# Kernel optimization log

Hardware: AMD Instinct MI355X
Metric: run time of the kernel (lower is better)

The kernel has to match this reference:

```python
import jax, jax.numpy as jnp
import numpy as np

N_NODES = 100000
N_EDGES = 600000
PRE = 128
NEXT = 128


def setup_inputs() -> dict:
    key = jax.random.key(0)
    k1, k2, k3, k4, k5, k6 = jax.random.split(key, 6)
    node_embedding = jax.random.normal(k1, (N_NODES, PRE), dtype=jnp.float32)
    edges = jax.random.randint(k2, (N_EDGES, 2), 0, N_NODES, dtype=jnp.int64)
    # Linear weights use torch convention [out, in]; scale ~ He-ish for sanity.
    s = 1.0 / np.sqrt(PRE)
    W_left = jax.random.normal(k3, (NEXT, PRE), dtype=jnp.float32) * s
    W_right = jax.random.normal(k4, (NEXT, PRE), dtype=jnp.float32) * s
    W_update = jax.random.normal(k5, (NEXT, PRE), dtype=jnp.float32) * s
    b_update = jax.random.normal(k6, (NEXT,), dtype=jnp.float32) * s
    return {
        "node_embedding": node_embedding,
        "edges": edges,
        "W_left": W_left,
        "W_right": W_right,
        "W_update": W_update,
        "b_update": b_update,
        "next_size": NEXT,
    }


def reference(node_embedding, edges, W_left, W_right, W_update, b_update, next_size):
    # Vectorized form of the per-edge loop:
    #   for each edge (i0, i1):
    #     lg  = sigmoid(W_l @ x[i0])
    #     rg  = sigmoid(W_r @ x[i1])
    #     mid = tanh(W_u @ (x[i0] + x[i1]) + b)
    #     out = lg*mid + rg*mid
    x0 = node_embedding[edges[:, 0]]  # [E, pre]
    x1 = node_embedding[edges[:, 1]]  # [E, pre]
    lg = jax.nn.sigmoid(jnp.einsum("ep,np->en", x0, W_left))
    rg = jax.nn.sigmoid(jnp.einsum("ep,np->en", x1, W_right))
    mid = jnp.tanh(jnp.einsum("ep,np->en", x0 + x1, W_update) + b_update)
    return (lg + rg) * mid  # [E, next]
```

## Files before the change

kernel.cpp:

```cpp
#include <hip/hip_runtime.h>
#include <hip/hip_bf16.h>

typedef __attribute__((ext_vector_type(8))) short short8;
typedef __attribute__((ext_vector_type(4))) float f32x4;

__device__ __forceinline__ float bflo(unsigned int u) { return __uint_as_float(u << 16); }
__device__ __forceinline__ float bfhi(unsigned int u) { return __uint_as_float(u & 0xffff0000u); }
__device__ __forceinline__ unsigned int bfrne(float f) {
    unsigned int u = __float_as_uint(f);
    return (u + 0x7fffu + ((u >> 16) & 1u)) >> 16;
}
__device__ __forceinline__ unsigned int packbf2(float lo, float hi) {
    return (bfrne(lo) & 0xffffu) | (bfrne(hi) << 16);
}
__device__ __forceinline__ float fast_rcp(float x) { return __builtin_amdgcn_rcpf(x); }
__device__ __forceinline__ float sigmoidf_fast(float x) { return fast_rcp(1.0f + __expf(-x)); }
__device__ __forceinline__ float tanhf_fast(float x) {
    float e = __expf(2.0f * x);
    return 1.0f - 2.0f * fast_rcp(e + 1.0f);
}
__device__ __forceinline__ short8 pack8(const float* f) {
    short8 r;
#pragma unroll
    for (int i = 0; i < 8; i += 2) {
        unsigned int p = packbf2(f[i], f[i + 1]);
        r[i] = (short)(p & 0xffffu);
        r[i + 1] = (short)(p >> 16);
    }
    return r;
}
__device__ __forceinline__ void unpack8(uint4 v, float* f) {
    const unsigned int* p = (const unsigned int*)&v;
#pragma unroll
    for (int j = 0; j < 4; ++j) { f[2 * j] = bflo(p[j]); f[2 * j + 1] = bfhi(p[j]); }
}

__global__ void sniff_kernel(const unsigned short* __restrict__ emb,
                             const int* __restrict__ e32, int* __restrict__ flags)
{
    __shared__ int s_f32, s_nz;
    const int t = threadIdx.x;
    if (t == 0) { s_f32 = 0; s_nz = 0; }
    __syncthreads();
    int bad = 0;
#pragma unroll 4
    for (int j = 0; j < 64; ++j) {
        unsigned int u = emb[t * 64 + j];
        if (((u >> 7) & 0xFFu) == 0xFFu) bad = 1;
    }
    int nz = 0;
#pragma unroll
    for (int j = 0; j < 8; ++j)
        if (e32[(t * 8 + j) * 2 + 1] != 0) nz = 1;
    if (bad) atomicOr(&s_f32, 1);
    if (nz) atomicOr(&s_nz, 1);
    __syncthreads();
    if (t == 0) { flags[0] = s_f32; flags[1] = s_nz ? 0 : 1; }
}

__global__ __launch_bounds__(256, 2)
void proj_kernel(const void* __restrict__ embv,
                 const void* __restrict__ w0v, const void* __restrict__ w1v,
                 const void* __restrict__ w2v,
                 unsigned short* __restrict__ SLp,
                 unsigned short* __restrict__ SRp,
                 float* __restrict__ Up,
                 const int* __restrict__ flags, int n_nodes)
{
    const int in_f32 = flags[0];
    const int w = blockIdx.y;
    const void* Wv = (w == 0) ? w0v : (w == 1 ? w1v : w2v);
    const int m0 = blockIdx.x * 128;

    __shared__ unsigned short lds[128 * 136];

    const int tid  = threadIdx.x;
    const int lane = tid & 63;
    const int wave = tid >> 6;
    const int wm   = wave & 1;
    const int wn   = wave >> 1;
    const int l15  = lane & 15;
    const int lgp  = lane >> 4;

    short8 bf[4][4];
    if (in_f32) {
        const float* W = (const float*)Wv;
#pragma unroll
        for (int nj = 0; nj < 4; ++nj) {
            const float* wrow = W + (size_t)(wn * 64 + nj * 16 + l15) * 128 + lgp * 8;
#pragma unroll
            for (int s = 0; s < 4; ++s) {
                float f[8];
                *(uint4*)&f[0] = *(const uint4*)(wrow + s * 32);
                *(uint4*)&f[4] = *(const uint4*)(wrow + s * 32 + 4);
                bf[s][nj] = pack8(f);
            }
        }
    } else {
        const unsigned short* W = (const unsigned short*)Wv;
#pragma unroll
        for (int nj = 0; nj < 4; ++nj) {
            const unsigned short* wrow = W + (size_t)(wn * 64 + nj * 16 + l15) * 128 + lgp * 8;
#pragma unroll
            for (int s = 0; s < 4; ++s)
                bf[s][nj] = *(const short8*)(wrow + s * 32);
        }
    }

    if (in_f32) {
        const float* emb = (const float*)embv;
#pragma unroll
        for (int it = 0; it < 8; ++it) {
            int i = tid + it * 256;
            int row = i >> 4, ch = i & 15;
            int g = m0 + row;
            float f[8] = {0.f, 0.f, 0.f, 0.f, 0.f, 0.f, 0.f, 0.f};
            if (g < n_nodes) {
                const float* src = emb + (size_t)g * 128 + ch * 8;
                *(uint4*)&f[0] = *(const uint4*)src;
                *(uint4*)&f[4] = *(const uint4*)(src + 4);
            }
            *(short8*)(&lds[row * 136 + ch * 8]) = pack8(f);
        }
    } else {
        const unsigned short* emb = (const unsigned short*)embv;
#pragma unroll
        for (int it = 0; it < 4; ++it) {
            int i = tid + it * 256;
            int row = i >> 3, ch = i & 7;
            int g = m0 + row;
            uint4 v = make_uint4(0u, 0u, 0u, 0u);
            if (g < n_nodes) v = *(const uint4*)(emb + (size_t)g * 128 + ch * 8);
            *(uint4*)(&lds[row * 136 + ch * 8]) = v;
        }
    }

    f32x4 acc[4][4];
#pragma unroll
    for (int mi = 0; mi < 4; ++mi)
#pragma unroll
        for (int nj = 0; nj < 4; ++nj)
            acc[mi][nj] = (f32x4){0.f, 0.f, 0.f, 0.f};

    __syncthreads();

#pragma unroll
    for (int s = 0; s < 4; ++s) {
        short8 af[4];
#pragma unroll
        for (int mi = 0; mi < 4; ++mi)
            af[mi] = *(const short8*)(&lds[(wm * 64 + mi * 16 + l15) * 136 + s * 32 + lgp * 8]);
#pragma unroll
        for (int mi = 0; mi < 4; ++mi)
#pragma unroll
            for (int nj = 0; nj < 4; ++nj)
                acc[mi][nj] = __builtin_amdgcn_mfma_f32_16x16x32_bf16(
                    af[mi], bf[s][nj], acc[mi][nj], 0, 0, 0);
    }

    if (w < 2) {
        unsigned short* out = (w == 0) ? SLp : SRp;
        const bool odd = (lane & 1);
#pragma unroll
        for (int mi = 0; mi < 4; ++mi) {
            int nodeBase = m0 + wm * 64 + mi * 16 + lgp * 4;
#pragma unroll
            for (int nj = 0; nj < 4; ++nj) {
                float v0 = sigmoidf_fast(acc[mi][nj][0]);
                float v1 = sigmoidf_fast(acc[mi][nj][1]);
                float v2 = sigmoidf_fast(acc[mi][nj][2]);
                float v3 = sigmoidf_fast(acc[mi][nj][3]);
                float p0 = __shfl_xor(v0, 1), p1 = __shfl_xor(v1, 1);
                float p2 = __shfl_xor(v2, 1), p3 = __shfl_xor(v3, 1);
                unsigned int pkA, pkB; int rA, rB;
                if (!odd) { pkA = packbf2(v0, p0); rA = 0; pkB = packbf2(v1, p1); rB = 1; }
                else      { pkA = packbf2(p2, v2); rA = 2; pkB = packbf2(p3, v3); rB = 3; }
                int colE = wn * 64 + nj * 16 + (l15 & ~1);
                int na = nodeBase + rA, nb = nodeBase + rB;
                if (na < n_nodes) *(unsigned int*)(out + (size_t)na * 128 + colE) = pkA;
                if (nb < n_nodes) *(unsigned int*)(out + (size_t)nb * 128 + colE) = pkB;
            }
        }
    } else {
#pragma unroll
        for (int mi = 0; mi < 4; ++mi) {
            int nodeBase = m0 + wm * 64 + mi * 16 + lgp * 4;
#pragma unroll
            for (int nj = 0; nj < 4; ++nj) {
                int col = wn * 64 + nj * 16 + l15;
#pragma unroll
                for (int r = 0; r < 4; ++r) {
                    int row = nodeBase + r;
                    if (row < n_nodes) Up[(size_t)row * 128 + col] = acc[mi][nj][r];
                }
            }
        }
    }
}

__global__ __launch_bounds__(256)
void edge_kernel(const int* __restrict__ e32,
                 const unsigned short* __restrict__ SL,
                 const unsigned short* __restrict__ SR,
                 const float* __restrict__ U,
                 const void* __restrict__ biasv,
                 void* __restrict__ outv,
                 const int* __restrict__ flags, int n_edges)
{
    const int in_f32 = flags[0];
    const int i64    = flags[1];
    const int tid = threadIdx.x;
    const int e = blockIdx.x * 16 + (tid >> 4);
    if (e >= n_edges) return;
    const int c = (tid & 15) * 8;

    int a, b;
    if (i64) { a = e32[4 * (size_t)e]; b = e32[4 * (size_t)e + 2]; }
    else     { a = e32[2 * (size_t)e]; b = e32[2 * (size_t)e + 1]; }

    float slf[8], srf[8], uaf[8], ubf[8], bif[8];
    unpack8(*(const uint4*)(SL + (size_t)a * 128 + c), slf);
    unpack8(*(const uint4*)(SR + (size_t)b * 128 + c), srf);
    const float* ua = U + (size_t)a * 128 + c;
    const float* ub = U + (size_t)b * 128 + c;
    *(uint4*)&uaf[0] = *(const uint4*)ua;
    *(uint4*)&uaf[4] = *(const uint4*)(ua + 4);
    *(uint4*)&ubf[0] = *(const uint4*)ub;
    *(uint4*)&ubf[4] = *(const uint4*)(ub + 4);
    if (in_f32) {
        const float* bp = (const float*)biasv + c;
        *(uint4*)&bif[0] = *(const uint4*)bp;
        *(uint4*)&bif[4] = *(const uint4*)(bp + 4);
    } else {
        unpack8(*(const uint4*)((const unsigned short*)biasv + c), bif);
    }

    float o[8];
#pragma unroll
    for (int j = 0; j < 8; ++j) {
        float s = slf[j] + srf[j];
        float x = uaf[j] + ubf[j] + bif[j];
        o[j] = s * tanhf_fast(x);
    }

    if (in_f32) {
        float* op = (float*)outv + (size_t)e * 128 + c;
        *(uint4*)op = *(const uint4*)&o[0];
        *(uint4*)(op + 4) = *(const uint4*)&o[4];
    } else {
        unsigned int res[4];
#pragma unroll
        for (int j = 0; j < 4; ++j) res[j] = packbf2(o[2 * j], o[2 * j + 1]);
        *(uint4*)((unsigned short*)outv + (size_t)e * 128 + c) = *(const uint4*)res;
    }
}

extern "C" void kernel_launch(void* const* d_in, const int* in_sizes, int n_in,
                              void* d_out, int out_size, void* d_ws, size_t ws_size,
                              hipStream_t stream)
{
    const void* emb   = d_in[0];
    const int*  edges = (const int*)d_in[1];
    const void* Wl    = d_in[2];
    const void* Wr    = d_in[3];
    const void* Wu    = d_in[4];
    const void* bias  = d_in[5];

    const int n_nodes = in_sizes[0] / 128;
    const int n_edges = in_sizes[1] / 2;

    int* flags = (int*)d_ws;
    const size_t plane_elems = (size_t)n_nodes * 128;
    unsigned short* SLp = (unsigned short*)((char*)d_ws + 256);
    unsigned short* SRp = SLp + plane_elems;
    float*          Up  = (float*)(SRp + plane_elems);

    sniff_kernel<<<1, 256, 0, stream>>>((const unsigned short*)emb, edges, flags);

    dim3 g1((n_nodes + 127) / 128, 3);
    proj_kernel<<<g1, 256, 0, stream>>>(emb, Wl, Wr, Wu, SLp, SRp, Up, flags, n_nodes);

    int g2 = (n_edges + 15) / 16;
    edge_kernel<<<g2, 256, 0, stream>>>(edges, SLp, SRp, Up, bias, d_out, flags, n_edges);
}
```

Baseline: 511.1 us.

## Store U plane in fp16, fuse three projections per block, split-bf16 activations

```diff
diff --git a/kernel.cpp b/kernel.cpp
--- a/kernel.cpp
+++ b/kernel.cpp
@@ -1,5 +1,6 @@
 #include <hip/hip_runtime.h>
 #include <hip/hip_bf16.h>
+#include <hip/hip_fp16.h>
 
 typedef __attribute__((ext_vector_type(8))) short short8;
 typedef __attribute__((ext_vector_type(4))) float f32x4;
@@ -13,26 +14,41 @@
 __device__ __forceinline__ unsigned int packbf2(float lo, float hi) {
     return (bfrne(lo) & 0xffffu) | (bfrne(hi) << 16);
 }
+__device__ __forceinline__ short8 pack8(const float* f) {
+    short8 r;
+#pragma unroll
+    for (int i = 0; i < 8; i += 2) {
+        unsigned int p = packbf2(f[i], f[i + 1]);
+        r[i] = (short)(p & 0xffffu);
+        r[i + 1] = (short)(p >> 16);
+    }
+    return r;
+}
+__device__ __forceinline__ void unpackbf8(uint4 v, float* f) {
+    const unsigned int* p = (const unsigned int*)&v;
+#pragma unroll
+    for (int j = 0; j < 4; ++j) { f[2 * j] = bflo(p[j]); f[2 * j + 1] = bfhi(p[j]); }
+}
+
+__device__ __forceinline__ unsigned int packh2(float lo, float hi) {
+    unsigned int a = __half_as_ushort(__float2half_rn(lo));
+    unsigned int b = __half_as_ushort(__float2half_rn(hi));
+    return a | (b << 16);
+}
+__device__ __forceinline__ void unpackh8(uint4 v, float* f) {
+    const unsigned int* p = (const unsigned int*)&v;
+#pragma unroll
+    for (int j = 0; j < 4; ++j) {
+        f[2 * j]     = __half2float(__ushort_as_half((unsigned short)(p[j] & 0xffffu)));
+        f[2 * j + 1] = __half2float(__ushort_as_half((unsigned short)(p[j] >> 16)));
+    }
+}
+
 __device__ __forceinline__ float fast_rcp(float x) { return __builtin_amdgcn_rcpf(x); }
 __device__ __forceinline__ float sigmoidf_fast(float x) { return fast_rcp(1.0f + __expf(-x)); }
 __device__ __forceinline__ float tanhf_fast(float x) {
     float e = __expf(2.0f * x);
     return 1.0f - 2.0f * fast_rcp(e + 1.0f);
-}
-__device__ __forceinline__ short8 pack8(const float* f) {
-    short8 r;
-#pragma unroll
-    for (int i = 0; i < 8; i += 2) {
-        unsigned int p = packbf2(f[i], f[i + 1]);
-        r[i] = (short)(p & 0xffffu);
-        r[i + 1] = (short)(p >> 16);
-    }
-    return r;
-}
-__device__ __forceinline__ void unpack8(uint4 v, float* f) {
-    const unsigned int* p = (const unsigned int*)&v;
-#pragma unroll
-    for (int j = 0; j < 4; ++j) { f[2 * j] = bflo(p[j]); f[2 * j + 1] = bfhi(p[j]); }
 }
 
 __global__ void sniff_kernel(const unsigned short* __restrict__ emb,
@@ -58,21 +74,49 @@
     if (t == 0) { flags[0] = s_f32; flags[1] = s_nz ? 0 : 1; }
 }
 
+__global__ __launch_bounds__(256)
+void prep_kernel(const void* __restrict__ w0v, const void* __restrict__ w1v,
+                 const void* __restrict__ w2v,
+                 unsigned short* __restrict__ Wb, const int* __restrict__ flags)
+{
+    const int in_f32 = flags[0];
+    const int w = blockIdx.x;
+    const void* Wv = (w == 0) ? w0v : (w == 1 ? w1v : w2v);
+    unsigned short* dst = Wb + w * 16384;
+    const int tid = threadIdx.x;
+    if (in_f32) {
+        const float* W = (const float*)Wv;
+#pragma unroll
+        for (int it = 0; it < 8; ++it) {
+            int i = (tid + it * 256) * 8;
+            float f[8];
+            *(uint4*)&f[0] = *(const uint4*)(W + i);
+            *(uint4*)&f[4] = *(const uint4*)(W + i + 4);
+            *(short8*)(dst + i) = pack8(f);
+        }
+    } else {
+        const unsigned short* W = (const unsigned short*)Wv;
+#pragma unroll
+        for (int it = 0; it < 8; ++it) {
+            int i = (tid + it * 256) * 8;
+            *(uint4*)(dst + i) = *(const uint4*)(W + i);
+        }
+    }
+}
+
 __global__ __launch_bounds__(256, 2)
 void proj_kernel(const void* __restrict__ embv,
-                 const void* __restrict__ w0v, const void* __restrict__ w1v,
-                 const void* __restrict__ w2v,
+                 const unsigned short* __restrict__ Wb,
                  unsigned short* __restrict__ SLp,
                  unsigned short* __restrict__ SRp,
-                 float* __restrict__ Up,
+                 unsigned short* __restrict__ Up,
                  const int* __restrict__ flags, int n_nodes)
 {
     const int in_f32 = flags[0];
-    const int w = blockIdx.y;
-    const void* Wv = (w == 0) ? w0v : (w == 1 ? w1v : w2v);
     const int m0 = blockIdx.x * 128;
 
-    __shared__ unsigned short lds[128 * 136];
+    __shared__ unsigned short ldsh[128 * 136];
+    __shared__ unsigned short ldsl[128 * 136];
 
     const int tid  = threadIdx.x;
     const int lane = tid & 63;
@@ -81,31 +125,6 @@
     const int wn   = wave >> 1;
     const int l15  = lane & 15;
     const int lgp  = lane >> 4;
-
-    short8 bf[4][4];
-    if (in_f32) {
-        const float* W = (const float*)Wv;
-#pragma unroll
-        for (int nj = 0; nj < 4; ++nj) {
-            const float* wrow = W + (size_t)(wn * 64 + nj * 16 + l15) * 128 + lgp * 8;
-#pragma unroll
-            for (int s = 0; s < 4; ++s) {
-                float f[8];
-                *(uint4*)&f[0] = *(const uint4*)(wrow + s * 32);
-                *(uint4*)&f[4] = *(const uint4*)(wrow + s * 32 + 4);
-                bf[s][nj] = pack8(f);
-            }
-        }
-    } else {
-        const unsigned short* W = (const unsigned short*)Wv;
-#pragma unroll
-        for (int nj = 0; nj < 4; ++nj) {
-            const unsigned short* wrow = W + (size_t)(wn * 64 + nj * 16 + l15) * 128 + lgp * 8;
-#pragma unroll
-            for (int s = 0; s < 4; ++s)
-                bf[s][nj] = *(const short8*)(wrow + s * 32);
-        }
-    }
 
     if (in_f32) {
         const float* emb = (const float*)embv;
@@ -120,7 +139,16 @@
                 *(uint4*)&f[0] = *(const uint4*)src;
                 *(uint4*)&f[4] = *(const uint4*)(src + 4);
             }
-            *(short8*)(&lds[row * 136 + ch * 8]) = pack8(f);
+            short8 h, l;
+#pragma unroll
+            for (int j = 0; j < 8; ++j) {
+                unsigned int uh = bfrne(f[j]);
+                h[j] = (short)uh;
+                float r = f[j] - __uint_as_float(uh << 16);
+                l[j] = (short)bfrne(r);
+            }
+            *(short8*)(&ldsh[row * 136 + ch * 8]) = h;
+            *(short8*)(&ldsl[row * 136 + ch * 8]) = l;
         }
     } else {
         const unsigned short* emb = (const unsigned short*)embv;
@@ -131,70 +159,85 @@
             int g = m0 + row;
             uint4 v = make_uint4(0u, 0u, 0u, 0u);
             if (g < n_nodes) v = *(const uint4*)(emb + (size_t)g * 128 + ch * 8);
-            *(uint4*)(&lds[row * 136 + ch * 8]) = v;
-        }
-    }
-
-    f32x4 acc[4][4];
-#pragma unroll
-    for (int mi = 0; mi < 4; ++mi)
-#pragma unroll
-        for (int nj = 0; nj < 4; ++nj)
-            acc[mi][nj] = (f32x4){0.f, 0.f, 0.f, 0.f};
+            *(uint4*)(&ldsh[row * 136 + ch * 8]) = v;
+        }
+    }
 
     __syncthreads();
 
-#pragma unroll
-    for (int s = 0; s < 4; ++s) {
-        short8 af[4];
+#pragma unroll 1
+    for (int w = 0; w < 3; ++w) {
+        const unsigned short* Wp = Wb + w * 16384;
+
+        short8 bf[4][4];
+#pragma unroll
+        for (int nj = 0; nj < 4; ++nj) {
+            const unsigned short* wrow = Wp + (size_t)(wn * 64 + nj * 16 + l15) * 128 + lgp * 8;
+#pragma unroll
+            for (int s = 0; s < 4; ++s)
+                bf[s][nj] = *(const short8*)(wrow + s * 32);
+        }
+
+        f32x4 acc[4][4];
 #pragma unroll
         for (int mi = 0; mi < 4; ++mi)
-            af[mi] = *(const short8*)(&lds[(wm * 64 + mi * 16 + l15) * 136 + s * 32 + lgp * 8]);
-#pragma unroll
-        for (int mi = 0; mi < 4; ++mi)
 #pragma unroll
             for (int nj = 0; nj < 4; ++nj)
-                acc[mi][nj] = __builtin_amdgcn_mfma_f32_16x16x32_bf16(
-                    af[mi], bf[s][nj], acc[mi][nj], 0, 0, 0);
-    }
-
-    if (w < 2) {
-        unsigned short* out = (w == 0) ? SLp : SRp;
+                acc[mi][nj] = (f32x4){0.f, 0.f, 0.f, 0.f};
+
+#pragma unroll
+        for (int s = 0; s < 4; ++s) {
+            short8 afh[4];
+#pragma unroll
+            for (int mi = 0; mi < 4; ++mi)
+                afh[mi] = *(const short8*)(&ldsh[(wm * 64 + mi * 16 + l15) * 136 + s * 32 + lgp * 8]);
+#pragma unroll
+            for (int mi = 0; mi < 4; ++mi)
+#pragma unroll
+                for (int nj = 0; nj < 4; ++nj)
+                    acc[mi][nj] = __builtin_amdgcn_mfma_f32_16x16x32_bf16(
+                        afh[mi], bf[s][nj], acc[mi][nj], 0, 0, 0);
+            if (in_f32) {
+                short8 afl[4];
+#pragma unroll
+                for (int mi = 0; mi < 4; ++mi)
+                    afl[mi] = *(const short8*)(&ldsl[(wm * 64 + mi * 16 + l15) * 136 + s * 32 + lgp * 8]);
+#pragma unroll
+                for (int mi = 0; mi < 4; ++mi)
+#pragma unroll
+                    for (int nj = 0; nj < 4; ++nj)
+                        acc[mi][nj] = __builtin_amdgcn_mfma_f32_16x16x32_bf16(
+                            afl[mi], bf[s][nj], acc[mi][nj], 0, 0, 0);
+            }
+        }
+
+        unsigned short* out = (w == 0) ? SLp : (w == 1 ? SRp : Up);
+        const bool gate = (w < 2);
         const bool odd = (lane & 1);
 #pragma unroll
         for (int mi = 0; mi < 4; ++mi) {
             int nodeBase = m0 + wm * 64 + mi * 16 + lgp * 4;
 #pragma unroll
             for (int nj = 0; nj < 4; ++nj) {
-                float v0 = sigmoidf_fast(acc[mi][nj][0]);
-                float v1 = sigmoidf_fast(acc[mi][nj][1]);
-                float v2 = sigmoidf_fast(acc[mi][nj][2]);
-                float v3 = sigmoidf_fast(acc[mi][nj][3]);
+                float v0 = acc[mi][nj][0];
+                float v1 = acc[mi][nj][1];
+                float v2 = acc[mi][nj][2];
+                float v3 = acc[mi][nj][3];
+                if (gate) {
+                    v0 = sigmoidf_fast(v0); v1 = sigmoidf_fast(v1);
+                    v2 = sigmoidf_fast(v2); v3 = sigmoidf_fast(v3);
+                }
                 float p0 = __shfl_xor(v0, 1), p1 = __shfl_xor(v1, 1);
                 float p2 = __shfl_xor(v2, 1), p3 = __shfl_xor(v3, 1);
                 unsigned int pkA, pkB; int rA, rB;
-                if (!odd) { pkA = packbf2(v0, p0); rA = 0; pkB = packbf2(v1, p1); rB = 1; }
-                else      { pkA = packbf2(p2, v2); rA = 2; pkB = packbf2(p3, v3); rB = 3; }
+                if (!odd) { pkA = packh2(v0, p0); rA = 0; pkB = packh2(v1, p1); rB = 1; }
+                else      { pkA = packh2(p2, v2); rA = 2; pkB = packh2(p3, v3); rB = 3; }
                 int colE = wn * 64 + nj * 16 + (l15 & ~1);
                 int na = nodeBase + rA, nb = nodeBase + rB;
                 if (na < n_nodes) *(unsigned int*)(out + (size_t)na * 128 + colE) = pkA;
                 if (nb < n_nodes) *(unsigned int*)(out + (size_t)nb * 128 + colE) = pkB;
             }
         }
-    } else {
-#pragma unroll
-        for (int mi = 0; mi < 4; ++mi) {
-            int nodeBase = m0 + wm * 64 + mi * 16 + lgp * 4;
-#pragma unroll
-            for (int nj = 0; nj < 4; ++nj) {
-                int col = wn * 64 + nj * 16 + l15;
-#pragma unroll
-                for (int r = 0; r < 4; ++r) {
-                    int row = nodeBase + r;
-                    if (row < n_nodes) Up[(size_t)row * 128 + col] = acc[mi][nj][r];
-                }
-            }
-        }
     }
 }
 
@@ -202,7 +245,7 @@
 void edge_kernel(const int* __restrict__ e32,
                  const unsigned short* __restrict__ SL,
                  const unsigned short* __restrict__ SR,
-                 const float* __restrict__ U,
+                 const unsigned short* __restrict__ U,
                  const void* __restrict__ biasv,
                  void* __restrict__ outv,
                  const int* __restrict__ flags, int n_edges)
@@ -215,24 +258,20 @@
     const int c = (tid & 15) * 8;
 
     int a, b;
-    if (i64) { a = e32[4 * (size_t)e]; b = e32[4 * (size_t)e + 2]; }
-    else     { a = e32[2 * (size_t)e]; b = e32[2 * (size_t)e + 1]; }
+    if (i64) { int4 ev = *(const int4*)(e32 + 4 * (size_t)e); a = ev.x; b = ev.z; }
+    else     { int2 ev = *(const int2*)(e32 + 2 * (size_t)e); a = ev.x; b = ev.y; }
 
     float slf[8], srf[8], uaf[8], ubf[8], bif[8];
-    unpack8(*(const uint4*)(SL + (size_t)a * 128 + c), slf);
-    unpack8(*(const uint4*)(SR + (size_t)b * 128 + c), srf);
-    const float* ua = U + (size_t)a * 128 + c;
-    const float* ub = U + (size_t)b * 128 + c;
-    *(uint4*)&uaf[0] = *(const uint4*)ua;
-    *(uint4*)&uaf[4] = *(const uint4*)(ua + 4);
-    *(uint4*)&ubf[0] = *(const uint4*)ub;
-    *(uint4*)&ubf[4] = *(const uint4*)(ub + 4);
+    unpackh8(*(const uint4*)(SL + (size_t)a * 128 + c), slf);
+    unpackh8(*(const uint4*)(SR + (size_t)b * 128 + c), srf);
+    unpackh8(*(const uint4*)(U  + (size_t)a * 128 + c), uaf);
+    unpackh8(*(const uint4*)(U  + (size_t)b * 128 + c), ubf);
     if (in_f32) {
         const float* bp = (const float*)biasv + c;
         *(uint4*)&bif[0] = *(const uint4*)bp;
         *(uint4*)&bif[4] = *(const uint4*)(bp + 4);
     } else {
-        unpack8(*(const uint4*)((const unsigned short*)biasv + c), bif);
+        unpackbf8(*(const uint4*)((const unsigned short*)biasv + c), bif);
     }
 
     float o[8];
@@ -270,15 +309,18 @@
     const int n_edges = in_sizes[1] / 2;
 
     int* flags = (int*)d_ws;
+    unsigned short* Wb = (unsigned short*)((char*)d_ws + 256);
     const size_t plane_elems = (size_t)n_nodes * 128;
-    unsigned short* SLp = (unsigned short*)((char*)d_ws + 256);
+    unsigned short* SLp = Wb + 3 * 16384;
     unsigned short* SRp = SLp + plane_elems;
-    float*          Up  = (float*)(SRp + plane_elems);
+    unsigned short* Up  = SRp + plane_elems;
 
     sniff_kernel<<<1, 256, 0, stream>>>((const unsigned short*)emb, edges, flags);
 
-    dim3 g1((n_nodes + 127) / 128, 3);
-    proj_kernel<<<g1, 256, 0, stream>>>(emb, Wl, Wr, Wu, SLp, SRp, Up, flags, n_nodes);
+    prep_kernel<<<3, 256, 0, stream>>>(Wl, Wr, Wu, Wb, flags);
+
+    dim3 g1((n_nodes + 127) / 128);
+    proj_kernel<<<g1, 256, 0, stream>>>(emb, Wb, SLp, SRp, Up, flags, n_nodes);
 
     int g2 = (n_edges + 15) / 16;
     edge_kernel<<<g2, 256, 0, stream>>>(edges, SLp, SRp, Up, bias, d_out, flags, n_edges);
```

Result: faster. 475.7 us (-6.9%).
